# Kernel tuning notes

Measured on AMD Instinct MI355X. Metric: run time of the kernel, lower is better.

The kernel has to match this reference:

```python
import jax, jax.numpy as jnp
import numpy as np

EPS = 1e-10


def setup_inputs() -> dict:
    key = jax.random.key(0)
    k1, k2 = jax.random.split(key)
    supports = jax.random.normal(k1, (32, 512, 1024), dtype=jnp.float32)
    targets = jax.random.normal(k2, (32, 512, 1024), dtype=jnp.float32)
    return {"supports": supports, "targets": targets}


def reference(supports, targets):
    # targets: [B, T, D], supports: [B, S, D] -> sim: [B, T, S]
    # F.cosine_similarity(a, b, eps): dot / max(||a||*||b||, eps)
    dots = jnp.einsum("btd,bsd->bts", targets, supports)
    t_norm = jnp.linalg.norm(targets, axis=-1)   # [B, T]
    s_norm = jnp.linalg.norm(supports, axis=-1)  # [B, S]
    denom = jnp.maximum(t_norm[:, :, None] * s_norm[:, None, :], EPS)
    sim = dots / denom
    # normalize=True default: map (-1, 1) -> (0, 1)
    return (sim + 1.0) * 0.5
```

## Files before the change

### kernel.cpp

```cpp
#include <hip/hip_runtime.h>
#include <hip/hip_bf16.h>

typedef __attribute__((ext_vector_type(8))) short short8;
typedef __attribute__((ext_vector_type(4))) float f32x4;

#define NBATCH 32
#define NT 512
#define NS 512
#define ND 1024
#define BM 128
#define BN 128
#define BK 64
#define NK (ND / BK)

__device__ __forceinline__ short f2bf(float f) {
    union { __hip_bfloat16 h; short s; } u;
    u.h = __float2bfloat16(f);
    return u.s;
}

__device__ __forceinline__ short8 cvt8(float4 a, float4 b) {
    short8 r;
    r[0] = f2bf(a.x); r[1] = f2bf(a.y); r[2] = f2bf(a.z); r[3] = f2bf(a.w);
    r[4] = f2bf(b.x); r[5] = f2bf(b.y); r[6] = f2bf(b.z); r[7] = f2bf(b.w);
    return r;
}

__device__ __forceinline__ float ssq4(float s, float4 a) {
    return fmaf(a.x, a.x, fmaf(a.y, a.y, fmaf(a.z, a.z, fmaf(a.w, a.w, s))));
}

__global__ __launch_bounds__(512, 4)
void paircos_mfma(const float* __restrict__ sup, const float* __restrict__ tgt,
                  float* __restrict__ out) {
    __shared__ __align__(16) short As[2][BM * BK];
    __shared__ __align__(16) short Bs[2][BN * BK];
    __shared__ float tn[BM];
    __shared__ float sn[BN];

    const int tid = threadIdx.x;
    const int l    = blockIdx.x;
    const int wgid = (l & 7) * 64 + (l >> 3);
    const int b    = wgid >> 4;
    const int til  = wgid & 15;
    const int bt0  = (til >> 2) * BM;
    const int bs0  = (til & 3) * BN;

    const int seg  = tid & 7;
    const int srow = tid >> 3;

    const float* gA = tgt + (size_t)b * NT * ND + (size_t)(bt0 + srow) * ND + seg * 8;
    const float* gB = sup + (size_t)b * NS * ND + (size_t)(bs0 + srow) * ND + seg * 8;

    const int wave = tid >> 6;
    const int lane = tid & 63;
    const int wr  = (wave >> 2) * 64;
    const int wc  = (wave & 3) * 32;
    const int lhi = lane >> 4;
    const int llo = lane & 15;

    f32x4 acc[4][2];
#pragma unroll
    for (int m = 0; m < 4; ++m)
#pragma unroll
        for (int n = 0; n < 2; ++n)
            acc[m][n] = (f32x4){0.f, 0.f, 0.f, 0.f};

    float sqa0 = 0.f, sqa1 = 0.f, sqb0 = 0.f, sqb1 = 0.f;

    float4 pA0, pA1, pA2, pA3, pB0, pB1, pB2, pB3;

    const int pu   = (seg ^ (srow & 7)) * 8;
    const int offw0 = srow * BK + pu;
    const int offw1 = (srow + 64) * BK + pu;

#define LOADT(KK)                                                              \
    do {                                                                       \
        pA0 = *reinterpret_cast<const float4*>(gA + (KK) * BK);                \
        pA1 = *reinterpret_cast<const float4*>(gA + (KK) * BK + 4);            \
        pA2 = *reinterpret_cast<const float4*>(gA + (KK) * BK + 64 * ND);      \
        pA3 = *reinterpret_cast<const float4*>(gA + (KK) * BK + 64 * ND + 4);  \
        pB0 = *reinterpret_cast<const float4*>(gB + (KK) * BK);                \
        pB1 = *reinterpret_cast<const float4*>(gB + (KK) * BK + 4);            \
        pB2 = *reinterpret_cast<const float4*>(gB + (KK) * BK + 64 * ND);      \
        pB3 = *reinterpret_cast<const float4*>(gB + (KK) * BK + 64 * ND + 4);  \
    } while (0)

#define STORET(P)                                                              \
    do {                                                                       \
        sqa0 = ssq4(ssq4(sqa0, pA0), pA1);                                     \
        *reinterpret_cast<short8*>(&As[P][offw0]) = cvt8(pA0, pA1);            \
        sqa1 = ssq4(ssq4(sqa1, pA2), pA3);                                     \
        *reinterpret_cast<short8*>(&As[P][offw1]) = cvt8(pA2, pA3);            \
        sqb0 = ssq4(ssq4(sqb0, pB0), pB1);                                     \
        *reinterpret_cast<short8*>(&Bs[P][offw0]) = cvt8(pB0, pB1);            \
        sqb1 = ssq4(ssq4(sqb1, pB2), pB3);                                     \
        *reinterpret_cast<short8*>(&Bs[P][offw1]) = cvt8(pB2, pB3);            \
    } while (0)

#define FRAG_READ(P, KS)                                                       \
    do {                                                                       \
        _Pragma("unroll") for (int m = 0; m < 4; ++m) {                        \
            const int row = wr + m * 16 + llo;                                 \
            const int off = row * BK + ((((KS) * 4 + lhi) ^ (row & 7)) * 8);   \
            af[m] = *reinterpret_cast<const short8*>(&As[P][off]);             \
        }                                                                      \
        _Pragma("unroll") for (int n = 0; n < 2; ++n) {                        \
            const int row = wc + n * 16 + llo;                                 \
            const int off = row * BK + ((((KS) * 4 + lhi) ^ (row & 7)) * 8);   \
            bfr[n] = *reinterpret_cast<const short8*>(&Bs[P][off]);            \
        }                                                                      \
    } while (0)

#define MFMA_BLOCK()                                                           \
    do {                                                                       \
        __builtin_amdgcn_s_setprio(1);                                         \
        _Pragma("unroll") for (int m = 0; m < 4; ++m)                          \
            _Pragma("unroll") for (int n = 0; n < 2; ++n)                      \
                acc[m][n] = __builtin_amdgcn_mfma_f32_16x16x32_bf16(           \
                    af[m], bfr[n], acc[m][n], 0, 0, 0);                        \
        __builtin_amdgcn_s_setprio(0);                                         \
    } while (0)

#define PHASE_FENCE()                                                          \
    do {                                                                       \
        asm volatile("s_waitcnt lgkmcnt(0)" ::: "memory");                     \
        __builtin_amdgcn_s_barrier();                                          \
        asm volatile("" ::: "memory");                                         \
    } while (0)

    LOADT(0);
    STORET(0);
    LOADT(1);
    PHASE_FENCE();

    for (int k = 0; k < NK; ++k) {
        const int cur = k & 1;
        short8 af[4], bfr[2];
        FRAG_READ(cur, 0);
        if (k + 1 < NK) STORET(cur ^ 1);
        if (k + 2 < NK) LOADT(k + 2);
        MFMA_BLOCK();
        FRAG_READ(cur, 1);
        MFMA_BLOCK();
        PHASE_FENCE();
    }

#pragma unroll
    for (int d = 1; d < 8; d <<= 1) {
        sqa0 += __shfl_xor(sqa0, d);
        sqa1 += __shfl_xor(sqa1, d);
        sqb0 += __shfl_xor(sqb0, d);
        sqb1 += __shfl_xor(sqb1, d);
    }
    if (seg == 0) {
        tn[srow]      = sqrtf(sqa0);
        tn[srow + 64] = sqrtf(sqa1);
        sn[srow]      = sqrtf(sqb0);
        sn[srow + 64] = sqrtf(sqb1);
    }
    __syncthreads();

    float* outp = out + (size_t)b * NT * NS;
#pragma unroll
    for (int m = 0; m < 4; ++m) {
        const int lr0 = wr + m * 16 + lhi * 4;
#pragma unroll
        for (int n = 0; n < 2; ++n) {
            const int lc = wc + n * 16 + llo;
            const float snv = sn[lc];
            const int col = bs0 + lc;
#pragma unroll
            for (int j = 0; j < 4; ++j) {
                const float denom = fmaxf(tn[lr0 + j] * snv, 1e-10f);
                outp[(size_t)(bt0 + lr0 + j) * NS + col] =
                    acc[m][n][j] / denom * 0.5f + 0.5f;
            }
        }
    }
}

extern "C" void kernel_launch(void* const* d_in, const int* in_sizes, int n_in,
                              void* d_out, int out_size, void* d_ws, size_t ws_size,
                              hipStream_t stream) {
    const float* sup = (const float*)d_in[0];
    const float* tgt = (const float*)d_in[1];
    float* out = (float*)d_out;
    (void)in_sizes; (void)n_in; (void)out_size; (void)d_ws; (void)ws_size;
    paircos_mfma<<<dim3(16 * NBATCH), 512, 0, stream>>>(sup, tgt, out);
}
```

Baseline: 40.53 us.

## Enlarge output tile to 128x256 with BK=32 and halve grid

Widens each workgroup's output tile from 128x128 to 128x256 and halves the K step to 32. Each wave now computes a 64x64 sub-tile with 16 accumulators, the LDS swizzle is reworked for the narrower rows, and the grid shrinks from 512 to 256 workgroups. The aim is more reuse of the target rows, which are now converted and read once per 256 support columns, cutting redundant global loads and fp32-to-bf16 conversions. In exchange there are twice as many K iterations and barriers, higher register pressure (launch bounds drop to 2), and only 256 workgroups to spread over the device's CUs.

```diff
diff --git a/kernel.cpp b/kernel.cpp
--- a/kernel.cpp
+++ b/kernel.cpp
@@ -9,8 +9,8 @@
 #define NS 512
 #define ND 1024
 #define BM 128
-#define BN 128
-#define BK 64
+#define BN 256
+#define BK 32
 #define NK (ND / BK)
 
 __device__ __forceinline__ short f2bf(float f) {
@@ -30,7 +30,7 @@
     return fmaf(a.x, a.x, fmaf(a.y, a.y, fmaf(a.z, a.z, fmaf(a.w, a.w, s))));
 }
 
-__global__ __launch_bounds__(512, 4)
+__global__ __launch_bounds__(512, 2)
 void paircos_mfma(const float* __restrict__ sup, const float* __restrict__ tgt,
                   float* __restrict__ out) {
     __shared__ __align__(16) short As[2][BM * BK];
@@ -40,14 +40,14 @@
 
     const int tid = threadIdx.x;
     const int l    = blockIdx.x;
-    const int wgid = (l & 7) * 64 + (l >> 3);
-    const int b    = wgid >> 4;
-    const int til  = wgid & 15;
-    const int bt0  = (til >> 2) * BM;
-    const int bs0  = (til & 3) * BN;
+    const int wgid = (l & 7) * 32 + (l >> 3);
+    const int b    = wgid >> 3;
+    const int til  = wgid & 7;
+    const int bt0  = (til >> 1) * BM;
+    const int bs0  = (til & 1) * BN;
 
-    const int seg  = tid & 7;
-    const int srow = tid >> 3;
+    const int seg  = tid & 3;
+    const int srow = tid >> 2;
 
     const float* gA = tgt + (size_t)b * NT * ND + (size_t)(bt0 + srow) * ND + seg * 8;
     const float* gB = sup + (size_t)b * NS * ND + (size_t)(bs0 + srow) * ND + seg * 8;
@@ -55,59 +55,54 @@
     const int wave = tid >> 6;
     const int lane = tid & 63;
     const int wr  = (wave >> 2) * 64;
-    const int wc  = (wave & 3) * 32;
+    const int wc  = (wave & 3) * 64;
     const int lhi = lane >> 4;
     const int llo = lane & 15;
 
-    f32x4 acc[4][2];
+    f32x4 acc[4][4];
 #pragma unroll
     for (int m = 0; m < 4; ++m)
 #pragma unroll
-        for (int n = 0; n < 2; ++n)
+        for (int n = 0; n < 4; ++n)
             acc[m][n] = (f32x4){0.f, 0.f, 0.f, 0.f};
 
-    float sqa0 = 0.f, sqa1 = 0.f, sqb0 = 0.f, sqb1 = 0.f;
+    float sqa = 0.f, sqb0 = 0.f, sqb1 = 0.f;
 
-    float4 pA0, pA1, pA2, pA3, pB0, pB1, pB2, pB3;
+    float4 pA0, pA1, pB0, pB1, pB2, pB3;
 
-    const int pu   = (seg ^ (srow & 7)) * 8;
-    const int offw0 = srow * BK + pu;
-    const int offw1 = (srow + 64) * BK + pu;
+    const int pu   = ((seg + (srow >> 1)) & 3) * 8;
+    const int offw = srow * BK + pu;
 
 #define LOADT(KK)                                                              \
     do {                                                                       \
         pA0 = *reinterpret_cast<const float4*>(gA + (KK) * BK);                \
         pA1 = *reinterpret_cast<const float4*>(gA + (KK) * BK + 4);            \
-        pA2 = *reinterpret_cast<const float4*>(gA + (KK) * BK + 64 * ND);      \
-        pA3 = *reinterpret_cast<const float4*>(gA + (KK) * BK + 64 * ND + 4);  \
         pB0 = *reinterpret_cast<const float4*>(gB + (KK) * BK);                \
         pB1 = *reinterpret_cast<const float4*>(gB + (KK) * BK + 4);            \
-        pB2 = *reinterpret_cast<const float4*>(gB + (KK) * BK + 64 * ND);      \
-        pB3 = *reinterpret_cast<const float4*>(gB + (KK) * BK + 64 * ND + 4);  \
+        pB2 = *reinterpret_cast<const float4*>(gB + (KK) * BK + 128 * ND);     \
+        pB3 = *reinterpret_cast<const float4*>(gB + (KK) * BK + 128 * ND + 4); \
     } while (0)
 
 #define STORET(P)                                                              \
     do {                                                                       \
-        sqa0 = ssq4(ssq4(sqa0, pA0), pA1);                                     \
-        *reinterpret_cast<short8*>(&As[P][offw0]) = cvt8(pA0, pA1);            \
-        sqa1 = ssq4(ssq4(sqa1, pA2), pA3);                                     \
-        *reinterpret_cast<short8*>(&As[P][offw1]) = cvt8(pA2, pA3);            \
+        sqa  = ssq4(ssq4(sqa,  pA0), pA1);                                     \
+        *reinterpret_cast<short8*>(&As[P][offw]) = cvt8(pA0, pA1);             \
         sqb0 = ssq4(ssq4(sqb0, pB0), pB1);                                     \
-        *reinterpret_cast<short8*>(&Bs[P][offw0]) = cvt8(pB0, pB1);            \
+        *reinterpret_cast<short8*>(&Bs[P][offw]) = cvt8(pB0, pB1);             \
         sqb1 = ssq4(ssq4(sqb1, pB2), pB3);                                     \
-        *reinterpret_cast<short8*>(&Bs[P][offw1]) = cvt8(pB2, pB3);            \
+        *reinterpret_cast<short8*>(&Bs[P][offw + 128 * BK]) = cvt8(pB2, pB3);  \
     } while (0)
 
-#define FRAG_READ(P, KS)                                                       \
+#define FRAG_READ(P)                                                           \
     do {                                                                       \
         _Pragma("unroll") for (int m = 0; m < 4; ++m) {                        \
             const int row = wr + m * 16 + llo;                                 \
-            const int off = row * BK + ((((KS) * 4 + lhi) ^ (row & 7)) * 8);   \
+            const int off = row * BK + (((lhi + (row >> 1)) & 3) * 8);         \
             af[m] = *reinterpret_cast<const short8*>(&As[P][off]);             \
         }                                                                      \
-        _Pragma("unroll") for (int n = 0; n < 2; ++n) {                        \
+        _Pragma("unroll") for (int n = 0; n < 4; ++n) {                        \
             const int row = wc + n * 16 + llo;                                 \
-            const int off = row * BK + ((((KS) * 4 + lhi) ^ (row & 7)) * 8);   \
+            const int off = row * BK + (((lhi + (row >> 1)) & 3) * 8);         \
             bfr[n] = *reinterpret_cast<const short8*>(&Bs[P][off]);            \
         }                                                                      \
     } while (0)
@@ -116,7 +111,7 @@
     do {                                                                       \
         __builtin_amdgcn_s_setprio(1);                                         \
         _Pragma("unroll") for (int m = 0; m < 4; ++m)                          \
-            _Pragma("unroll") for (int n = 0; n < 2; ++n)                      \
+            _Pragma("unroll") for (int n = 0; n < 4; ++n)                      \
                 acc[m][n] = __builtin_amdgcn_mfma_f32_16x16x32_bf16(           \
                     af[m], bfr[n], acc[m][n], 0, 0, 0);                        \
         __builtin_amdgcn_s_setprio(0);                                         \
@@ -136,28 +131,24 @@
 
     for (int k = 0; k < NK; ++k) {
         const int cur = k & 1;
-        short8 af[4], bfr[2];
-        FRAG_READ(cur, 0);
+        short8 af[4], bfr[4];
+        FRAG_READ(cur);
         if (k + 1 < NK) STORET(cur ^ 1);
         if (k + 2 < NK) LOADT(k + 2);
-        MFMA_BLOCK();
-        FRAG_READ(cur, 1);
         MFMA_BLOCK();
         PHASE_FENCE();
     }
 
-#pragma unroll
-    for (int d = 1; d < 8; d <<= 1) {
-        sqa0 += __shfl_xor(sqa0, d);
-        sqa1 += __shfl_xor(sqa1, d);
-        sqb0 += __shfl_xor(sqb0, d);
-        sqb1 += __shfl_xor(sqb1, d);
-    }
+    sqa  += __shfl_xor(sqa, 1);
+    sqa  += __shfl_xor(sqa, 2);
+    sqb0 += __shfl_xor(sqb0, 1);
+    sqb0 += __shfl_xor(sqb0, 2);
+    sqb1 += __shfl_xor(sqb1, 1);
+    sqb1 += __shfl_xor(sqb1, 2);
     if (seg == 0) {
-        tn[srow]      = sqrtf(sqa0);
-        tn[srow + 64] = sqrtf(sqa1);
-        sn[srow]      = sqrtf(sqb0);
-        sn[srow + 64] = sqrtf(sqb1);
+        tn[srow]       = sqrtf(sqa);
+        sn[srow]       = sqrtf(sqb0);
+        sn[srow + 128] = sqrtf(sqb1);
     }
     __syncthreads();
 
@@ -166,7 +157,7 @@
     for (int m = 0; m < 4; ++m) {
         const int lr0 = wr + m * 16 + lhi * 4;
 #pragma unroll
-        for (int n = 0; n < 2; ++n) {
+        for (int n = 0; n < 4; ++n) {
             const int lc = wc + n * 16 + llo;
             const float snv = sn[lc];
             const int col = bs0 + lc;
@@ -187,5 +178,5 @@
     const float* tgt = (const float*)d_in[1];
     float* out = (float*)d_out;
     (void)in_sizes; (void)n_in; (void)out_size; (void)d_ws; (void)ws_size;
-    paircos_mfma<<<dim3(16 * NBATCH), 512, 0, stream>>>(sup, tgt, out);
+    paircos_mfma<<<dim3(32 * 8), 512, 0, stream>>>(sup, tgt, out);
 }
```

Measured after the change: 35.15 us. 1.15x faster.
